# Kernel optimization log

Hardware: AMD Instinct MI355X
Metric: run time of the kernel (lower is better)

The kernel has to match this reference:

```python
import jax, jax.numpy as jnp
import numpy as np

B, T, F, U, M = 4096, 16, 512, 512, 8
OUT = 3
DELTA_T = 0.04

# ln_tau_table: tau starts at 1.0, multiplied by sqrt(10) each trace
_LN_TAU = np.log(1.0) + np.arange(M) * (0.5 * np.log(10.0))
LN_TAU = jnp.asarray(_LN_TAU, dtype=jnp.float32)          # (M,)
DECAY = jnp.exp(-DELTA_T / (jnp.exp(LN_TAU) + 1e-7))       # (M,)


def setup_inputs() -> dict:
    key = jax.random.key(0)
    ks = jax.random.split(key, 5)
    sc = 0.02
    return {
        "x": jax.random.normal(ks[0], (B, T, F), jnp.float32),
        "Wr": jax.random.normal(ks[1], (F + U, U * M), jnp.float32) * sc,
        "br": jnp.zeros((U * M,), jnp.float32),
        "Wq": jax.random.normal(ks[2], (F + U, U), jnp.float32) * sc,
        "bq": jnp.zeros((U,), jnp.float32),
        "Ws": jax.random.normal(ks[3], (F + U, U * M), jnp.float32) * sc,
        "bs": jnp.zeros((U * M,), jnp.float32),
        "Wo": jax.random.normal(ks[4], (U, OUT), jnp.float32) * sc,
        "bo": jnp.zeros((OUT,), jnp.float32),
    }


def _ctgru_forward(x, Wr, br, Wq, bq, Ws, bs, Wo, bo):
    def step(h_hat, xt):
        # h_hat: (B, U, M); xt: (B, F)
        h = h_hat.sum(axis=2)                              # (B, U)
        fused = jnp.concatenate([xt, h], axis=1)           # (B, F+U)
        ln_tau_r = (fused @ Wr + br).reshape(-1, U, M)
        r = jax.nn.softmax(-jnp.square(ln_tau_r - LN_TAU), axis=2)
        ctx = jnp.sum(r * h_hat, axis=2)                   # (B, U)
        q = jnp.tanh(jnp.concatenate([xt, ctx], axis=1) @ Wq + bq)[:, :, None]
        ln_tau_s = (fused @ Ws + bs).reshape(-1, U, M)
        s = jax.nn.softmax(-jnp.square(ln_tau_s - LN_TAU), axis=2)
        h_hat_next = ((1.0 - s) * h_hat + s * q) * DECAY   # (B, U, M)
        return h_hat_next, h_hat_next.sum(axis=2)          # carry, per-step hidden

    h0 = jnp.zeros((x.shape[0], U, M), x.dtype)
    _, hiddens = jax.lax.scan(step, h0, jnp.swapaxes(x, 0, 1))  # (T, B, U)
    hiddens = jnp.swapaxes(hiddens, 0, 1)                  # (B, T, U)
    return hiddens @ Wo + bo                               # (B, T, OUT)


def reference(x, Wr, br, Wq, bq, Ws, bs, Wo, bo):
    return _ctgru_forward(x, Wr, br, Wq, bq, Ws, bs, Wo, bo)
```

## Files before the change

### kernel.cpp

```cpp
#include <hip/hip_runtime.h>
#include <hip/hip_fp16.h>
#include <cmath>

#define Bdim 4096
#define Tdim 16
#define Fdim 512
#define Udim 512
#define Mdim 8
#define Kdim 1024
#define Ndim 8192

typedef __attribute__((ext_vector_type(8))) short bf16x8;
typedef __attribute__((ext_vector_type(4))) float f32x4;
typedef __attribute__((address_space(1))) const void* as1_cvp;
typedef __attribute__((address_space(3))) void* as3_vp;

__device__ __constant__ float c_lntau[8] = {
  0.0f, 1.15129254649702286f, 2.30258509299404572f, 3.45387763949106858f,
  4.60517018598809144f, 5.75646273248511430f, 6.90775527898213716f, 8.05904782547916002f
};
__device__ __constant__ float c_decay[8] = {
  0.96078944f, 0.98743055f, 0.99600799f, 0.99873589f,
  0.99960008f, 0.99987352f, 0.99996000f, 0.99998735f
};

__device__ __forceinline__ unsigned short f2bf(float f) {
  unsigned u = __float_as_uint(f);
  return (unsigned short)((u + 0x7fffu + ((u >> 16) & 1u)) >> 16);
}
__device__ __forceinline__ void cvt_store8(float4 a, float4 b, short* ph, short* pl) {
  float f[8] = {a.x, a.y, a.z, a.w, b.x, b.y, b.z, b.w};
  bf16x8 hv, lv;
#pragma unroll
  for (int j = 0; j < 8; ++j) {
    unsigned short h = f2bf(f[j]);
    hv[j] = (short)h;
    float r = f[j] - __uint_as_float((unsigned)h << 16);
    lv[j] = (short)f2bf(r);
  }
  *(bf16x8*)ph = hv;
  *(bf16x8*)pl = lv;
}

#define GLOAD16(gp, lp) __builtin_amdgcn_global_load_lds((as1_cvp)(gp), (as3_vp)(lp), 16, 0, 0)

__global__ __launch_bounds__(256)
void wconv(const float* __restrict__ W, int ldw,
           short* __restrict__ WT_hi, short* __restrict__ WT_lo, int n_off)
{
  __shared__ float tile[64][65];
  const int tid = threadIdx.x;
  const int n0 = blockIdx.x * 64, k0 = blockIdx.y * 64;
#pragma unroll 4
  for (int i = 0; i < 16; ++i) {
    const int kl = i * 4 + (tid >> 6), nl = tid & 63;
    tile[kl][nl] = W[(size_t)(k0 + kl) * ldw + (n0 + nl)];
  }
  __syncthreads();
#pragma unroll 4
  for (int i = 0; i < 16; ++i) {
    const int nl = i * 4 + (tid >> 6), kl = tid & 63;
    const float v = tile[kl][nl];
    const unsigned short h = f2bf(v);
    const float r = v - __uint_as_float((unsigned)h << 16);
    const size_t di = (size_t)(n_off + n0 + nl) * 1024 + (k0 + kl);
    WT_hi[di] = (short)h;
    WT_lo[di] = (short)f2bf(r);
  }
}

__global__ __launch_bounds__(256)
void gemm_rs_mfma(const float* __restrict__ x, const float* __restrict__ h, int has_h,
                  const short* __restrict__ WT_hi, const short* __restrict__ WT_lo,
                  const float* __restrict__ br, const float* __restrict__ bs,
                  const float* __restrict__ h_hat, float* __restrict__ ctx,
                  __half* __restrict__ sbuf, int t)
{
  __shared__ short Ah[128 * 32], Al[128 * 32], Bh[128 * 32], Bl[128 * 32];
  const int tid = threadIdx.x, lane = tid & 63, wid = tid >> 6;
  const int m0 = blockIdx.y * 128, n0 = blockIdx.x * 128;
  const int wm = wid >> 1, wn = wid & 1;

  const int s_row = tid >> 1, s_kb = (tid & 1) * 16;
  const float* xrow = x + ((size_t)(m0 + s_row) * Tdim + t) * Fdim;
  const float* hrow = h + (size_t)(m0 + s_row) * Udim;

  f32x4 acc[4][4];
#pragma unroll
  for (int i = 0; i < 4; ++i)
#pragma unroll
    for (int j = 0; j < 4; ++j) acc[i][j] = 0.0f;

  for (int k0 = 0; k0 < Kdim; k0 += 32) {
    float4 va0, va1, va2, va3;
    if (k0 < Fdim) {
      const float* s = xrow + k0 + s_kb;
      va0 = *(const float4*)s; va1 = *(const float4*)(s + 4);
      va2 = *(const float4*)(s + 8); va3 = *(const float4*)(s + 12);
    } else if (has_h) {
      const float* s = hrow + (k0 - Fdim) + s_kb;
      va0 = *(const float4*)s; va1 = *(const float4*)(s + 4);
      va2 = *(const float4*)(s + 8); va3 = *(const float4*)(s + 12);
    } else {
      va0 = va1 = va2 = va3 = make_float4(0.f, 0.f, 0.f, 0.f);
    }
    __syncthreads();
    cvt_store8(va0, va1, &Ah[s_row * 32 + s_kb],     &Al[s_row * 32 + s_kb]);
    cvt_store8(va2, va3, &Ah[s_row * 32 + s_kb + 8], &Al[s_row * 32 + s_kb + 8]);
#pragma unroll
    for (int i = 0; i < 2; ++i) {
      const int nrow = wid * 32 + i * 16;
      const size_t gb = ((size_t)(n0 + nrow + (lane >> 2)) * 1024 + k0) * 2 + (size_t)(lane & 3) * 16;
      GLOAD16((const char*)WT_hi + gb, (char*)Bh + nrow * 64);
      GLOAD16((const char*)WT_lo + gb, (char*)Bl + nrow * 64);
    }
    __syncthreads();
    const int kg = lane >> 4, fr = lane & 15;
    bf16x8 ah[4], al[4], bh[4], bl[4];
#pragma unroll
    for (int mi = 0; mi < 4; ++mi) {
      const int row = wm * 64 + mi * 16 + fr;
      ah[mi] = *(const bf16x8*)&Ah[row * 32 + kg * 8];
      al[mi] = *(const bf16x8*)&Al[row * 32 + kg * 8];
    }
#pragma unroll
    for (int nj = 0; nj < 4; ++nj) {
      const int row = wn * 64 + nj * 16 + fr;
      bh[nj] = *(const bf16x8*)&Bh[row * 32 + kg * 8];
      bl[nj] = *(const bf16x8*)&Bl[row * 32 + kg * 8];
    }
#pragma unroll
    for (int mi = 0; mi < 4; ++mi)
#pragma unroll
      for (int nj = 0; nj < 4; ++nj) {
        acc[mi][nj] = __builtin_amdgcn_mfma_f32_16x16x32_bf16(ah[mi], bh[nj], acc[mi][nj], 0, 0, 0);
        acc[mi][nj] = __builtin_amdgcn_mfma_f32_16x16x32_bf16(ah[mi], bl[nj], acc[mi][nj], 0, 0, 0);
        acc[mi][nj] = __builtin_amdgcn_mfma_f32_16x16x32_bf16(al[mi], bh[nj], acc[mi][nj], 0, 0, 0);
      }
  }

  const bool is_s = (n0 >= Udim * Mdim);
  const float* bias = is_s ? bs : br;
  const int nb = is_s ? n0 - Udim * Mdim : n0;
  const float lnt = c_lntau[lane & 7];
  float bv[4];
#pragma unroll
  for (int nj = 0; nj < 4; ++nj) bv[nj] = bias[nb + wn * 64 + nj * 16 + (lane & 15)];

#pragma unroll
  for (int mi = 0; mi < 4; ++mi)
#pragma unroll
    for (int nj = 0; nj < 4; ++nj)
#pragma unroll
      for (int r = 0; r < 4; ++r) {
        const int brow = m0 + wm * 64 + mi * 16 + (lane >> 4) * 4 + r;
        const int ncol = nb + wn * 64 + nj * 16 + (lane & 15);
        const float v = acc[mi][nj][r] + bv[nj];
        const float d = v - lnt;
        float z = -d * d;
        float zm = z;
        zm = fmaxf(zm, __shfl_xor(zm, 1));
        zm = fmaxf(zm, __shfl_xor(zm, 2));
        zm = fmaxf(zm, __shfl_xor(zm, 4));
        const float e = expf(z - zm);
        float den = e;
        den += __shfl_xor(den, 1);
        den += __shfl_xor(den, 2);
        den += __shfl_xor(den, 4);
        const int u = ncol >> 3;
        if (!is_s) {
          const float hh = h_hat[((size_t)brow * Udim + u) * Mdim + (lane & 7)];
          float num = e * hh;
          num += __shfl_xor(num, 1);
          num += __shfl_xor(num, 2);
          num += __shfl_xor(num, 4);
          if ((lane & 7) == 0) ctx[(size_t)brow * Udim + u] = num / den;
        } else {
          sbuf[((size_t)brow * Udim + u) * Mdim + (lane & 7)] = __float2half(e / den);
        }
      }
}

__global__ __launch_bounds__(256)
void gemm_q_mfma(const float* __restrict__ x, const float* __restrict__ ctx,
                 const short* __restrict__ WqT_hi, const short* __restrict__ WqT_lo,
                 const float* __restrict__ bq, const __half* __restrict__ sbuf,
                 float* __restrict__ h_hat, float* __restrict__ hbuf, int t)
{
  __shared__ short Ah[64 * 32], Al[64 * 32], Bh[128 * 32], Bl[128 * 32];
  const int tid = threadIdx.x, lane = tid & 63, wid = tid >> 6;
  const int m0 = blockIdx.y * 64, n0 = blockIdx.x * 128;
  const int wm = wid >> 1, wn = wid & 1;

  const int s_row = tid >> 2, s_kb = (tid & 3) * 8;
  const float* xrow = x + ((size_t)(m0 + s_row) * Tdim + t) * Fdim;
  const float* crow = ctx + (size_t)(m0 + s_row) * Udim;

  f32x4 acc[2][4];
#pragma unroll
  for (int i = 0; i < 2; ++i)
#pragma unroll
    for (int j = 0; j < 4; ++j) acc[i][j] = 0.0f;

  for (int k0 = 0; k0 < Kdim; k0 += 32) {
    float4 va0, va1;
    if (k0 < Fdim) {
      const float* s = xrow + k0 + s_kb;
      va0 = *(const float4*)s; va1 = *(const float4*)(s + 4);
    } else {
      const float* s = crow + (k0 - Fdim) + s_kb;
      va0 = *(const float4*)s; va1 = *(const float4*)(s + 4);
    }
    __syncthreads();
    cvt_store8(va0, va1, &Ah[s_row * 32 + s_kb], &Al[s_row * 32 + s_kb]);
#pragma unroll
    for (int i = 0; i < 2; ++i) {
      const int nrow = wid * 32 + i * 16;
      const size_t gb = ((size_t)(n0 + nrow + (lane >> 2)) * 1024 + k0) * 2 + (size_t)(lane & 3) * 16;
      GLOAD16((const char*)WqT_hi + gb, (char*)Bh + nrow * 64);
      GLOAD16((const char*)WqT_lo + gb, (char*)Bl + nrow * 64);
    }
    __syncthreads();
    const int kg = lane >> 4, fr = lane & 15;
    bf16x8 ah[2], al[2], bh[4], bl[4];
#pragma unroll
    for (int mi = 0; mi < 2; ++mi) {
      const int row = wm * 32 + mi * 16 + fr;
      ah[mi] = *(const bf16x8*)&Ah[row * 32 + kg * 8];
      al[mi] = *(const bf16x8*)&Al[row * 32 + kg * 8];
    }
#pragma unroll
    for (int nj = 0; nj < 4; ++nj) {
      const int row = wn * 64 + nj * 16 + fr;
      bh[nj] = *(const bf16x8*)&Bh[row * 32 + kg * 8];
      bl[nj] = *(const bf16x8*)&Bl[row * 32 + kg * 8];
    }
#pragma unroll
    for (int mi = 0; mi < 2; ++mi)
#pragma unroll
      for (int nj = 0; nj < 4; ++nj) {
        acc[mi][nj] = __builtin_amdgcn_mfma_f32_16x16x32_bf16(ah[mi], bh[nj], acc[mi][nj], 0, 0, 0);
        acc[mi][nj] = __builtin_amdgcn_mfma_f32_16x16x32_bf16(ah[mi], bl[nj], acc[mi][nj], 0, 0, 0);
        acc[mi][nj] = __builtin_amdgcn_mfma_f32_16x16x32_bf16(al[mi], bh[nj], acc[mi][nj], 0, 0, 0);
      }
  }

  float bv[4];
#pragma unroll
  for (int nj = 0; nj < 4; ++nj) bv[nj] = bq[n0 + wn * 64 + nj * 16 + (lane & 15)];

#pragma unroll
  for (int mi = 0; mi < 2; ++mi)
#pragma unroll
    for (int nj = 0; nj < 4; ++nj)
#pragma unroll
      for (int r = 0; r < 4; ++r) {
        const int b = m0 + wm * 32 + mi * 16 + (lane >> 4) * 4 + r;
        const int u = n0 + wn * 64 + nj * 16 + (lane & 15);
        const float qv = tanhf(acc[mi][nj][r] + bv[nj]);
        const size_t base = ((size_t)b * Udim + u) * Mdim;
        const __half2* sp = (const __half2*)(sbuf + base);
        const __half2 s01 = sp[0], s23 = sp[1], s45 = sp[2], s67 = sp[3];
        float sv[8] = {__low2float(s01), __high2float(s01), __low2float(s23), __high2float(s23),
                       __low2float(s45), __high2float(s45), __low2float(s67), __high2float(s67)};
        const float4 h0 = *(const float4*)(h_hat + base);
        const float4 h1 = *(const float4*)(h_hat + base + 4);
        float hv[8] = {h0.x, h0.y, h0.z, h0.w, h1.x, h1.y, h1.z, h1.w};
        float sum = 0.f;
#pragma unroll
        for (int m = 0; m < 8; ++m) {
          const float nh = ((1.0f - sv[m]) * hv[m] + sv[m] * qv) * c_decay[m];
          hv[m] = nh;
          sum += nh;
        }
        *(float4*)(h_hat + base)     = make_float4(hv[0], hv[1], hv[2], hv[3]);
        *(float4*)(h_hat + base + 4) = make_float4(hv[4], hv[5], hv[6], hv[7]);
        hbuf[(size_t)b * Udim + u] = sum;
      }
}

__global__ __launch_bounds__(64)
void out_step(const float* __restrict__ h, const float* __restrict__ Wo,
              const float* __restrict__ bo, float* __restrict__ out, int t)
{
  const int b = blockIdx.x;
  const int lane = threadIdx.x;
  const float* hr = h + (size_t)b * Udim;
  float a0 = 0.f, a1 = 0.f, a2 = 0.f;
#pragma unroll
  for (int u0 = 0; u0 < Udim; u0 += 64) {
    const float hv = hr[u0 + lane];
    const float* w = Wo + (size_t)(u0 + lane) * 3;
    a0 = fmaf(hv, w[0], a0);
    a1 = fmaf(hv, w[1], a1);
    a2 = fmaf(hv, w[2], a2);
  }
#pragma unroll
  for (int off = 32; off; off >>= 1) {
    a0 += __shfl_down(a0, off);
    a1 += __shfl_down(a1, off);
    a2 += __shfl_down(a2, off);
  }
  if (lane == 0) {
    float* o = out + ((size_t)b * Tdim + t) * 3;
    o[0] = a0 + bo[0]; o[1] = a1 + bo[1]; o[2] = a2 + bo[2];
  }
}

__global__ __launch_bounds__(256)
void zero_kernel(float4* __restrict__ p, size_t n4)
{
  const size_t i = (size_t)blockIdx.x * 256 + threadIdx.x;
  const size_t stride = (size_t)gridDim.x * 256;
  for (size_t j = i; j < n4; j += stride)
    p[j] = make_float4(0.f, 0.f, 0.f, 0.f);
}

extern "C" void kernel_launch(void* const* d_in, const int* in_sizes, int n_in,
                              void* d_out, int out_size, void* d_ws, size_t ws_size,
                              hipStream_t stream)
{
  const float* x  = (const float*)d_in[0];
  const float* Wr = (const float*)d_in[1];
  const float* br = (const float*)d_in[2];
  const float* Wq = (const float*)d_in[3];
  const float* bq = (const float*)d_in[4];
  const float* Ws = (const float*)d_in[5];
  const float* bs = (const float*)d_in[6];
  const float* Wo = (const float*)d_in[7];
  const float* bo = (const float*)d_in[8];
  float* out = (float*)d_out;

  const size_t need = 153092096;
  if (ws_size < need) return;

  char* p = (char*)d_ws;
  short* WT_hi  = (short*)p;               p += 16777216;
  short* WT_lo  = (short*)p;               p += 16777216;
  short* WqT_hi = (short*)p;               p += 1048576;
  short* WqT_lo = (short*)p;               p += 1048576;
  float* hhat   = (float*)p;               p += 67108864;
  __half* sbuf  = (__half*)p;              p += 33554432;
  float* h      = (float*)p;               p += 8388608;
  float* ctx    = (float*)p;               p += 8388608;

  zero_kernel<<<4096, 256, 0, stream>>>((float4*)hhat, (size_t)Bdim * Udim * Mdim / 4);

  wconv<<<dim3(64, 16), 256, 0, stream>>>(Wr, 4096, WT_hi, WT_lo, 0);
  wconv<<<dim3(64, 16), 256, 0, stream>>>(Ws, 4096, WT_hi, WT_lo, 4096);
  wconv<<<dim3(8, 16),  256, 0, stream>>>(Wq, 512,  WqT_hi, WqT_lo, 0);

  for (int t = 0; t < Tdim; ++t) {
    gemm_rs_mfma<<<dim3(64, 32), 256, 0, stream>>>(x, h, (t > 0) ? 1 : 0,
                                                   WT_hi, WT_lo, br, bs,
                                                   hhat, ctx, sbuf, t);
    gemm_q_mfma<<<dim3(4, 64), 256, 0, stream>>>(x, ctx, WqT_hi, WqT_lo, bq,
                                                 sbuf, hhat, h, t);
    out_step<<<Bdim, 64, 0, stream>>>(h, Wo, bo, out, t);
  }
}
```

Measured before the change: 6.715 ms.

## Pre-split activations into bf16 hi/lo buffers and load them via LDS DMA

Each step's A operand (x_t and the hidden state h) is now split into bf16 hi/lo once and stored in global memory. The producer kernels write it: out_step writes the next x_t and gemm_q writes h. Both GEMMs then fetch A with global_load_lds, so every N-tile block no longer reloads fp32 data and converts it again. The first step skips the recurrent half of K, and ctx is stored already split. In exchange, Wq is now converted inside every gemm_q block, a redundant per-block cost, and the extra workspace adds global traffic.

```diff
diff --git a/kernel.cpp b/kernel.cpp
--- a/kernel.cpp
+++ b/kernel.cpp
@@ -8,7 +8,6 @@
 #define Udim 512
 #define Mdim 8
 #define Kdim 1024
-#define Ndim 8192
 
 typedef __attribute__((ext_vector_type(8))) short bf16x8;
 typedef __attribute__((ext_vector_type(4))) float f32x4;
@@ -28,6 +27,9 @@
   unsigned u = __float_as_uint(f);
   return (unsigned short)((u + 0x7fffu + ((u >> 16) & 1u)) >> 16);
 }
+__device__ __forceinline__ float bf2f(unsigned short h) {
+  return __uint_as_float((unsigned)h << 16);
+}
 __device__ __forceinline__ void cvt_store8(float4 a, float4 b, short* ph, short* pl) {
   float f[8] = {a.x, a.y, a.z, a.w, b.x, b.y, b.z, b.w};
   bf16x8 hv, lv;
@@ -35,8 +37,7 @@
   for (int j = 0; j < 8; ++j) {
     unsigned short h = f2bf(f[j]);
     hv[j] = (short)h;
-    float r = f[j] - __uint_as_float((unsigned)h << 16);
-    lv[j] = (short)f2bf(r);
+    lv[j] = (short)f2bf(f[j] - bf2f(h));
   }
   *(bf16x8*)ph = hv;
   *(bf16x8*)pl = lv;
@@ -62,28 +63,40 @@
     const int nl = i * 4 + (tid >> 6), kl = tid & 63;
     const float v = tile[kl][nl];
     const unsigned short h = f2bf(v);
-    const float r = v - __uint_as_float((unsigned)h << 16);
     const size_t di = (size_t)(n_off + n0 + nl) * 1024 + (k0 + kl);
     WT_hi[di] = (short)h;
-    WT_lo[di] = (short)f2bf(r);
-  }
+    WT_lo[di] = (short)f2bf(v - bf2f(h));
+  }
+}
+
+__device__ __forceinline__ void xsplit_row(const float* x, short* Ahw, short* Alw,
+                                           int b, int t, int j)
+{
+  const float* s = x + ((size_t)b * Tdim + t) * Fdim + j * 8;
+  const float4 a = *(const float4*)s;
+  const float4 c = *(const float4*)(s + 4);
+  cvt_store8(a, c, Ahw + (size_t)b * Kdim + j * 8, Alw + (size_t)b * Kdim + j * 8);
+}
+
+__global__ __launch_bounds__(64)
+void xsplit0(const float* __restrict__ x, short* Ahw, short* Alw)
+{
+  xsplit_row(x, Ahw, Alw, blockIdx.x, 0, threadIdx.x);
 }
 
 __global__ __launch_bounds__(256)
-void gemm_rs_mfma(const float* __restrict__ x, const float* __restrict__ h, int has_h,
-                  const short* __restrict__ WT_hi, const short* __restrict__ WT_lo,
+void gemm_rs_mfma(const short* __restrict__ Ahg, const short* __restrict__ Alg,
+                  const short* __restrict__ WTh, const short* __restrict__ WTl,
                   const float* __restrict__ br, const float* __restrict__ bs,
-                  const float* __restrict__ h_hat, float* __restrict__ ctx,
-                  __half* __restrict__ sbuf, int t)
+                  const float* __restrict__ h_hat, short* __restrict__ Ch,
+                  short* __restrict__ Cl, __half* __restrict__ sbuf, int kmax)
 {
   __shared__ short Ah[128 * 32], Al[128 * 32], Bh[128 * 32], Bl[128 * 32];
   const int tid = threadIdx.x, lane = tid & 63, wid = tid >> 6;
   const int m0 = blockIdx.y * 128, n0 = blockIdx.x * 128;
   const int wm = wid >> 1, wn = wid & 1;
-
-  const int s_row = tid >> 1, s_kb = (tid & 1) * 16;
-  const float* xrow = x + ((size_t)(m0 + s_row) * Tdim + t) * Fdim;
-  const float* hrow = h + (size_t)(m0 + s_row) * Udim;
+  const int lrow16 = lane >> 2;
+  const int lcb = (lane & 3) * 16;
 
   f32x4 acc[4][4];
 #pragma unroll
@@ -91,28 +104,17 @@
 #pragma unroll
     for (int j = 0; j < 4; ++j) acc[i][j] = 0.0f;
 
-  for (int k0 = 0; k0 < Kdim; k0 += 32) {
-    float4 va0, va1, va2, va3;
-    if (k0 < Fdim) {
-      const float* s = xrow + k0 + s_kb;
-      va0 = *(const float4*)s; va1 = *(const float4*)(s + 4);
-      va2 = *(const float4*)(s + 8); va3 = *(const float4*)(s + 12);
-    } else if (has_h) {
-      const float* s = hrow + (k0 - Fdim) + s_kb;
-      va0 = *(const float4*)s; va1 = *(const float4*)(s + 4);
-      va2 = *(const float4*)(s + 8); va3 = *(const float4*)(s + 12);
-    } else {
-      va0 = va1 = va2 = va3 = make_float4(0.f, 0.f, 0.f, 0.f);
-    }
+  for (int k0 = 0; k0 < kmax; k0 += 32) {
     __syncthreads();
-    cvt_store8(va0, va1, &Ah[s_row * 32 + s_kb],     &Al[s_row * 32 + s_kb]);
-    cvt_store8(va2, va3, &Ah[s_row * 32 + s_kb + 8], &Al[s_row * 32 + s_kb + 8]);
 #pragma unroll
     for (int i = 0; i < 2; ++i) {
-      const int nrow = wid * 32 + i * 16;
-      const size_t gb = ((size_t)(n0 + nrow + (lane >> 2)) * 1024 + k0) * 2 + (size_t)(lane & 3) * 16;
-      GLOAD16((const char*)WT_hi + gb, (char*)Bh + nrow * 64);
-      GLOAD16((const char*)WT_lo + gb, (char*)Bl + nrow * 64);
+      const int rb = wid * 32 + i * 16;
+      const size_t ga = ((size_t)(m0 + rb + lrow16) * Kdim + k0) * 2 + lcb;
+      GLOAD16((const char*)Ahg + ga, (char*)Ah + rb * 64);
+      GLOAD16((const char*)Alg + ga, (char*)Al + rb * 64);
+      const size_t gw = ((size_t)(n0 + rb + lrow16) * Kdim + k0) * 2 + lcb;
+      GLOAD16((const char*)WTh + gw, (char*)Bh + rb * 64);
+      GLOAD16((const char*)WTl + gw, (char*)Bl + rb * 64);
     }
     __syncthreads();
     const int kg = lane >> 4, fr = lane & 15;
@@ -174,7 +176,13 @@
           num += __shfl_xor(num, 1);
           num += __shfl_xor(num, 2);
           num += __shfl_xor(num, 4);
-          if ((lane & 7) == 0) ctx[(size_t)brow * Udim + u] = num / den;
+          if ((lane & 7) == 0) {
+            const float c = num / den;
+            const unsigned short chh = f2bf(c);
+            const size_t ci = (size_t)brow * Udim + u;
+            Ch[ci] = (short)chh;
+            Cl[ci] = (short)f2bf(c - bf2f(chh));
+          }
         } else {
           sbuf[((size_t)brow * Udim + u) * Mdim + (lane & 7)] = __float2half(e / den);
         }
@@ -182,19 +190,18 @@
 }
 
 __global__ __launch_bounds__(256)
-void gemm_q_mfma(const float* __restrict__ x, const float* __restrict__ ctx,
-                 const short* __restrict__ WqT_hi, const short* __restrict__ WqT_lo,
-                 const float* __restrict__ bq, const __half* __restrict__ sbuf,
-                 float* __restrict__ h_hat, float* __restrict__ hbuf, int t)
+void gemm_q_mfma(const short* Ahg, const short* Alg,
+                 const short* Chg, const short* Clg,
+                 const float* __restrict__ Wq, const float* __restrict__ bq,
+                 const __half* __restrict__ sbuf, float* __restrict__ h_hat,
+                 short* Ahw, short* Alw, int kmax)
 {
   __shared__ short Ah[64 * 32], Al[64 * 32], Bh[128 * 32], Bl[128 * 32];
   const int tid = threadIdx.x, lane = tid & 63, wid = tid >> 6;
   const int m0 = blockIdx.y * 64, n0 = blockIdx.x * 128;
   const int wm = wid >> 1, wn = wid & 1;
-
-  const int s_row = tid >> 2, s_kb = (tid & 3) * 8;
-  const float* xrow = x + ((size_t)(m0 + s_row) * Tdim + t) * Fdim;
-  const float* crow = ctx + (size_t)(m0 + s_row) * Udim;
+  const int lrow16 = lane >> 2, lcb = (lane & 3) * 16;
+  const int kr = tid & 31, ng = tid >> 5;
 
   f32x4 acc[2][4];
 #pragma unroll
@@ -202,23 +209,32 @@
 #pragma unroll
     for (int j = 0; j < 4; ++j) acc[i][j] = 0.0f;
 
-  for (int k0 = 0; k0 < Kdim; k0 += 32) {
-    float4 va0, va1;
-    if (k0 < Fdim) {
-      const float* s = xrow + k0 + s_kb;
-      va0 = *(const float4*)s; va1 = *(const float4*)(s + 4);
-    } else {
-      const float* s = crow + (k0 - Fdim) + s_kb;
-      va0 = *(const float4*)s; va1 = *(const float4*)(s + 4);
-    }
+  for (int k0 = 0; k0 < kmax; k0 += 32) {
     __syncthreads();
-    cvt_store8(va0, va1, &Ah[s_row * 32 + s_kb], &Al[s_row * 32 + s_kb]);
-#pragma unroll
-    for (int i = 0; i < 2; ++i) {
-      const int nrow = wid * 32 + i * 16;
-      const size_t gb = ((size_t)(n0 + nrow + (lane >> 2)) * 1024 + k0) * 2 + (size_t)(lane & 3) * 16;
-      GLOAD16((const char*)WqT_hi + gb, (char*)Bh + nrow * 64);
-      GLOAD16((const char*)WqT_lo + gb, (char*)Bl + nrow * 64);
+    {
+      const int rb = wid * 16;
+      if (k0 < Fdim) {
+        const size_t ga = ((size_t)(m0 + rb + lrow16) * Kdim + k0) * 2 + lcb;
+        GLOAD16((const char*)Ahg + ga, (char*)Ah + rb * 64);
+        GLOAD16((const char*)Alg + ga, (char*)Al + rb * 64);
+      } else {
+        const size_t ga = ((size_t)(m0 + rb + lrow16) * Udim + (k0 - Fdim)) * 2 + lcb;
+        GLOAD16((const char*)Chg + ga, (char*)Ah + rb * 64);
+        GLOAD16((const char*)Clg + ga, (char*)Al + rb * 64);
+      }
+    }
+    {
+      const float* wp = Wq + (size_t)(k0 + kr) * Udim + n0 + ng * 16;
+      const float4 w0 = *(const float4*)wp,      w1 = *(const float4*)(wp + 4);
+      const float4 w2 = *(const float4*)(wp + 8), w3 = *(const float4*)(wp + 12);
+      const float wv[16] = {w0.x, w0.y, w0.z, w0.w, w1.x, w1.y, w1.z, w1.w,
+                            w2.x, w2.y, w2.z, w2.w, w3.x, w3.y, w3.z, w3.w};
+#pragma unroll
+      for (int i2 = 0; i2 < 16; ++i2) {
+        const unsigned short hh = f2bf(wv[i2]);
+        Bh[(ng * 16 + i2) * 32 + kr] = (short)hh;
+        Bl[(ng * 16 + i2) * 32 + kr] = (short)f2bf(wv[i2] - bf2f(hh));
+      }
     }
     __syncthreads();
     const int kg = lane >> 4, fr = lane & 15;
@@ -261,8 +277,8 @@
         const size_t base = ((size_t)b * Udim + u) * Mdim;
         const __half2* sp = (const __half2*)(sbuf + base);
         const __half2 s01 = sp[0], s23 = sp[1], s45 = sp[2], s67 = sp[3];
-        float sv[8] = {__low2float(s01), __high2float(s01), __low2float(s23), __high2float(s23),
-                       __low2float(s45), __high2float(s45), __low2float(s67), __high2float(s67)};
+        const float sv[8] = {__low2float(s01), __high2float(s01), __low2float(s23), __high2float(s23),
+                             __low2float(s45), __high2float(s45), __low2float(s67), __high2float(s67)};
         const float4 h0 = *(const float4*)(h_hat + base);
         const float4 h1 = *(const float4*)(h_hat + base + 4);
         float hv[8] = {h0.x, h0.y, h0.z, h0.w, h1.x, h1.y, h1.z, h1.w};
@@ -275,22 +291,27 @@
         }
         *(float4*)(h_hat + base)     = make_float4(hv[0], hv[1], hv[2], hv[3]);
         *(float4*)(h_hat + base + 4) = make_float4(hv[4], hv[5], hv[6], hv[7]);
-        hbuf[(size_t)b * Udim + u] = sum;
+        const unsigned short sh = f2bf(sum);
+        Ahw[(size_t)b * Kdim + Fdim + u] = (short)sh;
+        Alw[(size_t)b * Kdim + Fdim + u] = (short)f2bf(sum - bf2f(sh));
       }
 }
 
 __global__ __launch_bounds__(64)
-void out_step(const float* __restrict__ h, const float* __restrict__ Wo,
-              const float* __restrict__ bo, float* __restrict__ out, int t)
-{
-  const int b = blockIdx.x;
-  const int lane = threadIdx.x;
-  const float* hr = h + (size_t)b * Udim;
+void out_step(const short* Ahg, const short* Alg,
+              const float* __restrict__ Wo, const float* __restrict__ bo,
+              float* __restrict__ out, const float* __restrict__ x,
+              short* Ahw, short* Alw, int t)
+{
+  const int b = blockIdx.x, lane = threadIdx.x;
+  const short* hh = Ahg + (size_t)b * Kdim + Fdim;
+  const short* hl = Alg + (size_t)b * Kdim + Fdim;
   float a0 = 0.f, a1 = 0.f, a2 = 0.f;
 #pragma unroll
   for (int u0 = 0; u0 < Udim; u0 += 64) {
-    const float hv = hr[u0 + lane];
-    const float* w = Wo + (size_t)(u0 + lane) * 3;
+    const int u = u0 + lane;
+    const float hv = bf2f((unsigned short)hh[u]) + bf2f((unsigned short)hl[u]);
+    const float* w = Wo + (size_t)u * 3;
     a0 = fmaf(hv, w[0], a0);
     a1 = fmaf(hv, w[1], a1);
     a2 = fmaf(hv, w[2], a2);
@@ -305,6 +326,7 @@
     float* o = out + ((size_t)b * Tdim + t) * 3;
     o[0] = a0 + bo[0]; o[1] = a1 + bo[1]; o[2] = a2 + bo[2];
   }
+  if (t + 1 < Tdim) xsplit_row(x, Ahw, Alw, b, t + 1, lane);
 }
 
 __global__ __launch_bounds__(256)
@@ -331,31 +353,30 @@
   const float* bo = (const float*)d_in[8];
   float* out = (float*)d_out;
 
-  const size_t need = 153092096;
+  const size_t need = 159383552;
   if (ws_size < need) return;
 
   char* p = (char*)d_ws;
-  short* WT_hi  = (short*)p;               p += 16777216;
-  short* WT_lo  = (short*)p;               p += 16777216;
-  short* WqT_hi = (short*)p;               p += 1048576;
-  short* WqT_lo = (short*)p;               p += 1048576;
-  float* hhat   = (float*)p;               p += 67108864;
-  __half* sbuf  = (__half*)p;              p += 33554432;
-  float* h      = (float*)p;               p += 8388608;
-  float* ctx    = (float*)p;               p += 8388608;
-
-  zero_kernel<<<4096, 256, 0, stream>>>((float4*)hhat, (size_t)Bdim * Udim * Mdim / 4);
-
-  wconv<<<dim3(64, 16), 256, 0, stream>>>(Wr, 4096, WT_hi, WT_lo, 0);
-  wconv<<<dim3(64, 16), 256, 0, stream>>>(Ws, 4096, WT_hi, WT_lo, 4096);
-  wconv<<<dim3(8, 16),  256, 0, stream>>>(Wq, 512,  WqT_hi, WqT_lo, 0);
+  short* WTh = (short*)p;  p += 16777216;
+  short* WTl = (short*)p;  p += 16777216;
+  short* Ahg = (short*)p;  p += 8388608;
+  short* Alg = (short*)p;  p += 8388608;
+  short* Ch  = (short*)p;  p += 4194304;
+  short* Cl  = (short*)p;  p += 4194304;
+  float* hhat = (float*)p; p += 67108864;
+  __half* sbuf = (__half*)p;
+
+  zero_kernel<<<2048, 256, 0, stream>>>((float4*)hhat, 4194304);
+  wconv<<<dim3(64, 16), 256, 0, stream>>>(Wr, 4096, WTh, WTl, 0);
+  wconv<<<dim3(64, 16), 256, 0, stream>>>(Ws, 4096, WTh, WTl, 4096);
+  xsplit0<<<4096, 64, 0, stream>>>(x, Ahg, Alg);
 
   for (int t = 0; t < Tdim; ++t) {
-    gemm_rs_mfma<<<dim3(64, 32), 256, 0, stream>>>(x, h, (t > 0) ? 1 : 0,
-                                                   WT_hi, WT_lo, br, bs,
-                                                   hhat, ctx, sbuf, t);
-    gemm_q_mfma<<<dim3(4, 64), 256, 0, stream>>>(x, ctx, WqT_hi, WqT_lo, bq,
-                                                 sbuf, hhat, h, t);
-    out_step<<<Bdim, 64, 0, stream>>>(h, Wo, bo, out, t);
-  }
-}
+    const int kmax = t ? Kdim : Fdim;
+    gemm_rs_mfma<<<dim3(64, 32), 256, 0, stream>>>(Ahg, Alg, WTh, WTl, br, bs,
+                                                   hhat, Ch, Cl, sbuf, kmax);
+    gemm_q_mfma<<<dim3(4, 64), 256, 0, stream>>>(Ahg, Alg, Ch, Cl, Wq, bq,
+                                                 sbuf, hhat, Ahg, Alg, kmax);
+    out_step<<<4096, 64, 0, stream>>>(Ahg, Alg, Wo, bo, out, x, Ahg, Alg, t);
+  }
+}
```

Result: no change. 6.619 ms (-1.4%).
